# Optimization experiments

Hardware: AMD Instinct MI355X
Metric: run time of the kernel (lower is better)

Reference implementation:

```python
import jax, jax.numpy as jnp
import numpy as np

H = 512  # hidden_size


def _xavier(key, shape):
    fan_out, fan_in = shape[0], shape[1]
    bound = jnp.sqrt(6.0 / (fan_in + fan_out)).astype(jnp.float32)
    return jax.random.uniform(key, shape, jnp.float32, -bound, bound)


def setup_inputs() -> dict:
    key = jax.random.key(0)
    ks = jax.random.split(key, 8)
    B, T, D = 256, 256, 64
    x = jax.random.normal(ks[0], (B, T, D), jnp.float32)
    # LSTM params, PyTorch layout: W_ih [4H, in], W_hh [4H, H], gate order i,f,g,o.
    # biases are zero-initialized in the module; b = b_ih + b_hh folded into one.
    W_ih_0 = _xavier(ks[1], (4 * H, D))
    W_hh_0 = _xavier(ks[2], (4 * H, H))
    b_0 = jnp.zeros((4 * H,), jnp.float32)
    W_ih_1 = _xavier(ks[3], (4 * H, H))
    W_hh_1 = _xavier(ks[4], (4 * H, H))
    b_1 = jnp.zeros((4 * H,), jnp.float32)
    # heads (PyTorch Linear default init: uniform(-1/sqrt(fan_in), 1/sqrt(fan_in)))
    def lin(k, out_f, in_f):
        kw, kb = jax.random.split(k)
        bound = 1.0 / np.sqrt(in_f)
        W = jax.random.uniform(kw, (out_f, in_f), jnp.float32, -bound, bound)
        b = jax.random.uniform(kb, (out_f,), jnp.float32, -bound, bound)
        return W, b
    W_sh, b_sh = lin(ks[5], H // 2, H)
    W_dir, b_dir = lin(ks[6], 1, H // 2)
    W_mag, b_mag = lin(ks[7], 1, H // 2)
    return {
        "x": x,
        "W_ih_0": W_ih_0, "W_hh_0": W_hh_0, "b_0": b_0,
        "W_ih_1": W_ih_1, "W_hh_1": W_hh_1, "b_1": b_1,
        "W_sh": W_sh, "b_sh": b_sh,
        "W_dir": W_dir, "b_dir": b_dir,
        "W_mag": W_mag, "b_mag": b_mag,
    }


def _lstm_layer(x, W_ih, W_hh, b):
    # x: [B, T, D] -> h_seq: [B, T, H]. Input projection batched over time.
    B = x.shape[0]
    xW = jnp.einsum('btd,gd->btg', x, W_ih) + b  # [B, T, 4H]
    xW = jnp.swapaxes(xW, 0, 1)                  # [T, B, 4H]

    def step(carry, xt):
        h, c = carry
        gates = xt + h @ W_hh.T                  # [B, 4H]
        i, f, g, o = jnp.split(gates, 4, axis=-1)
        i = jax.nn.sigmoid(i)
        f = jax.nn.sigmoid(f)
        g = jnp.tanh(g)
        o = jax.nn.sigmoid(o)
        c = f * c + i * g
        h = o * jnp.tanh(c)
        return (h, c), h

    h0 = jnp.zeros((B, H), x.dtype)
    c0 = jnp.zeros((B, H), x.dtype)
    _, h_seq = jax.lax.scan(step, (h0, c0), xW)  # [T, B, H]
    return jnp.swapaxes(h_seq, 0, 1)             # [B, T, H]


def reference(x, W_ih_0, W_hh_0, b_0, W_ih_1, W_hh_1, b_1,
              W_sh, b_sh, W_dir, b_dir, W_mag, b_mag):
    h1 = _lstm_layer(x, W_ih_0, W_hh_0, b_0)   # layer 0
    h2 = _lstm_layer(h1, W_ih_1, W_hh_1, b_1)  # layer 1 (dropout=0 / eval)
    last_hidden = jnp.mean(h2, axis=1)          # mean over time [B, H]
    out = jax.nn.relu(last_hidden @ W_sh.T + b_sh) * 1.5
    direction = out @ W_dir.T + b_dir           # [B, 1]
    magnitude = out @ W_mag.T + b_mag           # [B, 1]
    return (direction, magnitude)
```

## Files before the change

kernel.cpp:

```cpp
#include <hip/hip_runtime.h>
#include <hip/hip_bf16.h>

typedef __attribute__((ext_vector_type(8))) short v8s;
typedef __attribute__((ext_vector_type(4))) float v4f;

static_assert(sizeof(v8s) == 16, "v8s must be 16B");

constexpr int BATCH = 256;
constexpr int SEQT  = 256;
constexpr int HID   = 512;
constexpr int NSLICES = 64;
constexpr int KBH  = 16;
constexpr int KBI0 = 2;
constexpr int KBT0 = KBH + KBI0;
constexpr int KBI1 = 16;
constexpr int KBT1 = KBH + KBI1;
constexpr int BH   = BATCH * HID;


__device__ inline short f2bf(float f) {
    union { __hip_bfloat16 h; short s; } u;
    u.h = __float2bfloat16(f);
    return u.s;
}
__device__ inline float sigf(float x) { return 1.0f / (1.0f + __expf(-x)); }
__device__ inline float tanhf_fast(float x) { return 1.0f - 2.0f / (__expf(2.0f * x) + 1.0f); }

__device__ inline void ld16_wait(const void* p, v8s a[16]) {
    asm volatile(
        "global_load_dwordx4 %0, %16, off sc1\n\t"
        "global_load_dwordx4 %1, %16, off offset:64 sc1\n\t"
        "global_load_dwordx4 %2, %16, off offset:128 sc1\n\t"
        "global_load_dwordx4 %3, %16, off offset:192 sc1\n\t"
        "global_load_dwordx4 %4, %16, off offset:256 sc1\n\t"
        "global_load_dwordx4 %5, %16, off offset:320 sc1\n\t"
        "global_load_dwordx4 %6, %16, off offset:384 sc1\n\t"
        "global_load_dwordx4 %7, %16, off offset:448 sc1\n\t"
        "global_load_dwordx4 %8, %16, off offset:512 sc1\n\t"
        "global_load_dwordx4 %9, %16, off offset:576 sc1\n\t"
        "global_load_dwordx4 %10, %16, off offset:640 sc1\n\t"
        "global_load_dwordx4 %11, %16, off offset:704 sc1\n\t"
        "global_load_dwordx4 %12, %16, off offset:768 sc1\n\t"
        "global_load_dwordx4 %13, %16, off offset:832 sc1\n\t"
        "global_load_dwordx4 %14, %16, off offset:896 sc1\n\t"
        "global_load_dwordx4 %15, %16, off offset:960 sc1\n\t"
        "s_waitcnt vmcnt(0)"
        : "=&v"(a[0]), "=&v"(a[1]), "=&v"(a[2]), "=&v"(a[3]),
          "=&v"(a[4]), "=&v"(a[5]), "=&v"(a[6]), "=&v"(a[7]),
          "=&v"(a[8]), "=&v"(a[9]), "=&v"(a[10]), "=&v"(a[11]),
          "=&v"(a[12]), "=&v"(a[13]), "=&v"(a[14]), "=&v"(a[15])
        : "v"(p) : "memory");
}

__device__ inline void ld16_issue(const void* p, v8s a[16]) {
    asm volatile(
        "global_load_dwordx4 %0, %16, off sc1\n\t"
        "global_load_dwordx4 %1, %16, off offset:64 sc1\n\t"
        "global_load_dwordx4 %2, %16, off offset:128 sc1\n\t"
        "global_load_dwordx4 %3, %16, off offset:192 sc1\n\t"
        "global_load_dwordx4 %4, %16, off offset:256 sc1\n\t"
        "global_load_dwordx4 %5, %16, off offset:320 sc1\n\t"
        "global_load_dwordx4 %6, %16, off offset:384 sc1\n\t"
        "global_load_dwordx4 %7, %16, off offset:448 sc1\n\t"
        "global_load_dwordx4 %8, %16, off offset:512 sc1\n\t"
        "global_load_dwordx4 %9, %16, off offset:576 sc1\n\t"
        "global_load_dwordx4 %10, %16, off offset:640 sc1\n\t"
        "global_load_dwordx4 %11, %16, off offset:704 sc1\n\t"
        "global_load_dwordx4 %12, %16, off offset:768 sc1\n\t"
        "global_load_dwordx4 %13, %16, off offset:832 sc1\n\t"
        "global_load_dwordx4 %14, %16, off offset:896 sc1\n\t"
        "global_load_dwordx4 %15, %16, off offset:960 sc1"
        : "=&v"(a[0]), "=&v"(a[1]), "=&v"(a[2]), "=&v"(a[3]),
          "=&v"(a[4]), "=&v"(a[5]), "=&v"(a[6]), "=&v"(a[7]),
          "=&v"(a[8]), "=&v"(a[9]), "=&v"(a[10]), "=&v"(a[11]),
          "=&v"(a[12]), "=&v"(a[13]), "=&v"(a[14]), "=&v"(a[15])
        : "v"(p) : "memory");
}

__device__ inline void wait_vm0_bind(v8s a[16]) {
    asm volatile("s_waitcnt vmcnt(0)"
        : "+v"(a[0]), "+v"(a[1]), "+v"(a[2]), "+v"(a[3]),
          "+v"(a[4]), "+v"(a[5]), "+v"(a[6]), "+v"(a[7]),
          "+v"(a[8]), "+v"(a[9]), "+v"(a[10]), "+v"(a[11]),
          "+v"(a[12]), "+v"(a[13]), "+v"(a[14]), "+v"(a[15])
        :: "memory");
    __builtin_amdgcn_sched_barrier(0);
}

__device__ inline void st16(void* p, v8s v) {
    asm volatile("global_store_dwordx4 %0, %1, off sc1" :: "v"(p), "v"(v) : "memory");
}

__device__ inline int frags_not_ready(const v8s f[16]) {
    unsigned acc = 0xFFFFFFFFu;
#pragma unroll
    for (int kb = 0; kb < 16; ++kb) {
        union { v8s v; unsigned u[4]; } q; q.v = f[kb];
#pragma unroll
        for (int j = 0; j < 4; ++j) {
            unsigned tw = q.u[j] ^ 0xAAAAAAAAu;
            acc = (tw < acc) ? tw : acc;
        }
    }
    return acc == 0u;
}

__device__ inline void cell_update(const v4f& acc0, const v4f& acc1,
                                   float bi, float bf_, float bg_, float bo,
                                   bool lowhalf, float c[4], float hval[4]) {
    v4f sw0, sw1;
#pragma unroll
    for (int r = 0; r < 4; ++r) {
        sw0[r] = __shfl_xor(acc0[r], 8, 64);
        sw1[r] = __shfl_xor(acc1[r], 8, 64);
    }
#pragma unroll
    for (int r = 0; r < 4; ++r) {
        float ig = (lowhalf ? acc0[r] : sw0[r]) + bi;
        float fg = (lowhalf ? sw0[r] : acc0[r]) + bf_;
        float gg = (lowhalf ? acc1[r] : sw1[r]) + bg_;
        float og = (lowhalf ? sw1[r] : acc1[r]) + bo;
        float cv = sigf(fg) * c[r] + sigf(ig) * tanhf_fast(gg);
        c[r] = cv;
        hval[r] = sigf(og) * tanhf_fast(cv);
    }
}

__global__ __launch_bounds__(256, 1)
void lstm_fused(const float* __restrict__ x,
                const float* __restrict__ Wih0, const float* __restrict__ Whh0,
                const float* __restrict__ bias0,
                const float* __restrict__ Wih1, const float* __restrict__ Whh1,
                const float* __restrict__ bias1,
                float* mean_out,
                __hip_bfloat16* h0seq,
                __hip_bfloat16* ring4)
{
    __shared__ v8s ldsB0[2 * KBT0 * 64];
    __shared__ v8s ldsB1[2 * KBT1 * 64];
    __shared__ alignas(16) short stage[4][16][8];

    const int tid   = threadIdx.x;
    const int lane  = tid & 63;
    const int wv    = tid >> 6;
    const int slice = blockIdx.x & (NSLICES - 1);
    const int bg    = blockIdx.x >> 6;
    const int j0    = slice * 8;
    const int b0    = bg * 64;

    for (int idx = tid; idx < 2 * KBT0 * 64; idx += 256) {
        int tile = idx / (KBT0 * 64);
        int rem  = idx - tile * (KBT0 * 64);
        int kb   = rem >> 6;
        int ls   = rem & 63;
        int n    = tile * 16 + (ls & 15);
        int kh   = ls >> 4;
        int col  = (n >> 3) * 512 + j0 + (n & 7);
        int k    = kb * 32 + kh * 8;
        const float* src = (k < 512) ? (Whh0 + col * 512 + k)
                                     : (Wih0 + col * 64 + (k - 512));
        float4 f0 = ((const float4*)src)[0];
        float4 f1 = ((const float4*)src)[1];
        v8s b;
        b[0]=f2bf(f0.x); b[1]=f2bf(f0.y); b[2]=f2bf(f0.z); b[3]=f2bf(f0.w);
        b[4]=f2bf(f1.x); b[5]=f2bf(f1.y); b[6]=f2bf(f1.z); b[7]=f2bf(f1.w);
        ldsB0[idx] = b;
    }
    for (int idx = tid; idx < 2 * KBT1 * 64; idx += 256) {
        int tile = idx / (KBT1 * 64);
        int rem  = idx - tile * (KBT1 * 64);
        int kb   = rem >> 6;
        int ls   = rem & 63;
        int n    = tile * 16 + (ls & 15);
        int kh   = ls >> 4;
        int col  = (n >> 3) * 512 + j0 + (n & 7);
        int k    = kb * 32 + kh * 8;
        const float* src = (k < 512) ? (Whh1 + col * 512 + k)
                                     : (Wih1 + col * 512 + (k - 512));
        float4 f0 = ((const float4*)src)[0];
        float4 f1 = ((const float4*)src)[1];
        v8s b;
        b[0]=f2bf(f0.x); b[1]=f2bf(f0.y); b[2]=f2bf(f0.z); b[3]=f2bf(f0.w);
        b[4]=f2bf(f1.x); b[5]=f2bf(f1.y); b[6]=f2bf(f1.z); b[7]=f2bf(f1.w);
        ldsB1[idx] = b;
    }
    __syncthreads();

    const int m_a  = b0 + wv * 16 + (lane & 15);
    const int kh8  = (lane >> 4) * 8;
    const int jj   = lane & 7;
    const bool lowhalf = (lane & 8) == 0;
    const int rg   = lane >> 4;

    const float bi0 = bias0[0 * 512 + j0 + jj];
    const float bf0 = bias0[1 * 512 + j0 + jj];
    const float bg0 = bias0[2 * 512 + j0 + jj];
    const float bo0 = bias0[3 * 512 + j0 + jj];
    const float bi1 = bias1[0 * 512 + j0 + jj];
    const float bf1 = bias1[1 * 512 + j0 + jj];
    const float bg1 = bias1[2 * 512 + j0 + jj];
    const float bo1 = bias1[3 * 512 + j0 + jj];

    float c0[4]   = {0.f, 0.f, 0.f, 0.f};
    float c1[4]   = {0.f, 0.f, 0.f, 0.f};
    float hsum[4] = {0.f, 0.f, 0.f, 0.f};

    v8s pz;
#pragma unroll
    for (int i = 0; i < 8; ++i) pz[i] = (short)0xAAAA;

    for (int t = 0; t <= SEQT; ++t) {
        const bool doL0  = (t < SEQT);
        const int  s     = t - 1;
        const bool doL1  = (t > 0);
        const bool doL1r = doL1 && (s > 0);

        if (doL1 && lane < 16) {
            int bcell = b0 + wv * 16 + lane;
            st16(ring4 + (size_t)(t & 3) * BH + bcell * HID + j0, pz);
        }

        v8s fA0[16];
        const int tm1 = (t > 0) ? t - 1 : 0;
        const __hip_bfloat16* hp = h0seq + (size_t)tm1 * BH + m_a * HID + kh8;
        if (t > 0) ld16_issue(hp, fA0);

        v4f a00 = {0.f,0.f,0.f,0.f}, a01 = {0.f,0.f,0.f,0.f};
        if (doL0) {
#pragma unroll
            for (int kb = 0; kb < KBI0; ++kb) {
                const float* xp = x + (m_a * SEQT + t) * 64 + kb * 32 + kh8;
                float4 f0 = ((const float4*)xp)[0];
                float4 f1 = ((const float4*)xp)[1];
                v8s a;
                a[0]=f2bf(f0.x); a[1]=f2bf(f0.y); a[2]=f2bf(f0.z); a[3]=f2bf(f0.w);
                a[4]=f2bf(f1.x); a[5]=f2bf(f1.y); a[6]=f2bf(f1.z); a[7]=f2bf(f1.w);
                a00 = __builtin_amdgcn_mfma_f32_16x16x32_bf16(a, ldsB0[(KBH + kb) * 64 + lane], a00, 0, 0, 0);
                a01 = __builtin_amdgcn_mfma_f32_16x16x32_bf16(a, ldsB0[(KBT0 + KBH + kb) * 64 + lane], a01, 0, 0, 0);
            }
        }

        if (t > 0) {
            wait_vm0_bind(fA0);
            while (__any(frags_not_ready(fA0))) {
                __builtin_amdgcn_s_sleep(1);
                ld16_wait(hp, fA0);
            }
        }

        if (doL0) {
            if (t > 0) {
#pragma unroll
                for (int kb = 0; kb < KBH; ++kb) {
                    a00 = __builtin_amdgcn_mfma_f32_16x16x32_bf16(fA0[kb], ldsB0[kb * 64 + lane], a00, 0, 0, 0);
                    a01 = __builtin_amdgcn_mfma_f32_16x16x32_bf16(fA0[kb], ldsB0[(KBT0 + kb) * 64 + lane], a01, 0, 0, 0);
                }
            }
            float hval[4];
            cell_update(a00, a01, bi0, bf0, bg0, bo0, lowhalf, c0, hval);
            if (lowhalf) {
#pragma unroll
                for (int r = 0; r < 4; ++r)
                    stage[wv][rg * 4 + r][jj] = f2bf(hval[r]);
            }
            asm volatile("s_waitcnt lgkmcnt(0)" ::: "memory");
            if (lane < 16) {
                v8s row = *(const v8s*)(&stage[wv][lane][0]);
                int bcell = b0 + wv * 16 + lane;
                st16(h0seq + (size_t)t * BH + bcell * HID + j0, row);
            }
        }

        if (doL1) {
            v8s fA2[16];
            const __hip_bfloat16* rp = ring4 + (size_t)((s + 3) & 3) * BH + m_a * HID + kh8;
            if (doL1r) ld16_issue(rp, fA2);

            v4f a10 = {0.f,0.f,0.f,0.f}, a11 = {0.f,0.f,0.f,0.f};
#pragma unroll
            for (int kb = 0; kb < KBI1; ++kb) {
                a10 = __builtin_amdgcn_mfma_f32_16x16x32_bf16(fA0[kb], ldsB1[(KBH + kb) * 64 + lane], a10, 0, 0, 0);
                a11 = __builtin_amdgcn_mfma_f32_16x16x32_bf16(fA0[kb], ldsB1[(KBT1 + KBH + kb) * 64 + lane], a11, 0, 0, 0);
            }
            if (doL1r) {
                wait_vm0_bind(fA2);
                while (__any(frags_not_ready(fA2))) {
                    __builtin_amdgcn_s_sleep(1);
                    ld16_wait(rp, fA2);
                }
#pragma unroll
                for (int kb = 0; kb < KBH; ++kb) {
                    a10 = __builtin_amdgcn_mfma_f32_16x16x32_bf16(fA2[kb], ldsB1[kb * 64 + lane], a10, 0, 0, 0);
                    a11 = __builtin_amdgcn_mfma_f32_16x16x32_bf16(fA2[kb], ldsB1[(KBT1 + kb) * 64 + lane], a11, 0, 0, 0);
                }
            }
            float hval[4];
            cell_update(a10, a11, bi1, bf1, bg1, bo1, lowhalf, c1, hval);
#pragma unroll
            for (int r = 0; r < 4; ++r) hsum[r] += hval[r];
            if (lowhalf) {
#pragma unroll
                for (int r = 0; r < 4; ++r)
                    stage[wv][rg * 4 + r][jj] = f2bf(hval[r]);
            }
            asm volatile("s_waitcnt lgkmcnt(0)" ::: "memory");
            if (lane < 16) {
                int bcell = b0 + wv * 16 + lane;
                v8s row = *(const v8s*)(&stage[wv][lane][0]);
                st16(ring4 + (size_t)(s & 3) * BH + bcell * HID + j0, row);
            }
        }
    }

    if (lowhalf) {
        char* mb = (char*)mean_out;
#pragma unroll
        for (int r = 0; r < 4; ++r) {
            int bcell = b0 + wv * 16 + rg * 4 + r;
            int j = j0 + jj;
            float* dst = (float*)(mb + (size_t)(j >> 8) * 262144
                                     + (size_t)bcell * 1024 + (j & 255) * 4);
            *dst = hsum[r] * (1.0f / (float)SEQT);
        }
    }
}

__global__ __launch_bounds__(256)
void head_kernel(const float* __restrict__ mean_h,
                 const float* __restrict__ W_sh, const float* __restrict__ b_sh,
                 const float* __restrict__ W_dir, const float* __restrict__ b_dir,
                 const float* __restrict__ W_mag, const float* __restrict__ b_mag,
                 float* __restrict__ out)
{
    __shared__ float mh[512];
    __shared__ float red[256];
    const int b = blockIdx.x;
    const int tid = threadIdx.x;

    const char* mb = (const char*)mean_h;
    mh[tid]       = *(const float*)(mb + (size_t)b * 1024 + tid * 4);
    mh[tid + 256] = *(const float*)(mb + 262144 + (size_t)b * 1024 + tid * 4);
    __syncthreads();

    const float4* wrow = (const float4*)(W_sh + tid * 512);
    float dot = 0.f;
#pragma unroll 4
    for (int k4 = 0; k4 < 128; ++k4) {
        float4 w = wrow[k4];
        dot += w.x * mh[k4 * 4] + w.y * mh[k4 * 4 + 1]
             + w.z * mh[k4 * 4 + 2] + w.w * mh[k4 * 4 + 3];
    }
    float o = fmaxf(dot + b_sh[tid], 0.f) * 1.5f;

    red[tid] = o * W_dir[tid];
    __syncthreads();
    for (int s = 128; s > 0; s >>= 1) {
        if (tid < s) red[tid] += red[tid + s];
        __syncthreads();
    }
    if (tid == 0) out[b] = red[0] + b_dir[0];
    __syncthreads();

    red[tid] = o * W_mag[tid];
    __syncthreads();
    for (int s = 128; s > 0; s >>= 1) {
        if (tid < s) red[tid] += red[tid + s];
        __syncthreads();
    }
    if (tid == 0) out[256 + b] = red[0] + b_mag[0];
}

extern "C" void kernel_launch(void* const* d_in, const int* in_sizes, int n_in,
                              void* d_out, int out_size, void* d_ws, size_t ws_size,
                              hipStream_t stream) {
    const float* x    = (const float*)d_in[0];
    const float* Wih0 = (const float*)d_in[1];
    const float* Whh0 = (const float*)d_in[2];
    const float* b0   = (const float*)d_in[3];
    const float* Wih1 = (const float*)d_in[4];
    const float* Whh1 = (const float*)d_in[5];
    const float* b1   = (const float*)d_in[6];
    const float* Wsh  = (const float*)d_in[7];
    const float* bsh  = (const float*)d_in[8];
    const float* Wdir = (const float*)d_in[9];
    const float* bdir = (const float*)d_in[10];
    const float* Wmag = (const float*)d_in[11];
    const float* bmag = (const float*)d_in[12];

    char* ws = (char*)d_ws;
    __hip_bfloat16* ring4 = (__hip_bfloat16*)(ws);
    __hip_bfloat16* h0seq = (__hip_bfloat16*)(ws + 1048576);
    float* mean_h         = (float*)(ws + 1048576);


    lstm_fused<<<dim3(256), dim3(256), 0, stream>>>(
        x, Wih0, Whh0, b0, Wih1, Whh1, b1,
        mean_h, h0seq, ring4);
    head_kernel<<<dim3(256), dim3(256), 0, stream>>>(
        mean_h, Wsh, bsh, Wdir, bdir, Wmag, bmag, (float*)d_out);
}
```

Before: 1.462 ms.

## Prefetch next-step layer-0 hidden state and x inputs at end of iteration

```diff
diff --git a/kernel.cpp b/kernel.cpp
--- a/kernel.cpp
+++ b/kernel.cpp
@@ -209,29 +209,48 @@
 #pragma unroll
     for (int i = 0; i < 8; ++i) pz[i] = (short)0xAAAA;
 
+    v8s fP[16];
+    float4 xf[4];
+
+#pragma unroll
+    for (int kb = 0; kb < KBI0; ++kb) {
+        const float* xp = x + (m_a * SEQT + 0) * 64 + kb * 32 + kh8;
+        xf[kb * 2 + 0] = ((const float4*)xp)[0];
+        xf[kb * 2 + 1] = ((const float4*)xp)[1];
+    }
+
     for (int t = 0; t <= SEQT; ++t) {
         const bool doL0  = (t < SEQT);
         const int  s     = t - 1;
         const bool doL1  = (t > 0);
         const bool doL1r = doL1 && (s > 0);
 
-        if (doL1 && lane < 16) {
+        const __hip_bfloat16* hp = h0seq + (size_t)((t > 0) ? t - 1 : 0) * BH
+                                   + m_a * HID + kh8;
+        if (t > 0) {
+            wait_vm0_bind(fP);
+            while (__any(frags_not_ready(fP))) {
+                __builtin_amdgcn_s_sleep(1);
+                ld16_wait(hp, fP);
+            }
+        }
+
+        if (doL1 && doL0 && lane < 16) {
             int bcell = b0 + wv * 16 + lane;
             st16(ring4 + (size_t)(t & 3) * BH + bcell * HID + j0, pz);
         }
 
-        v8s fA0[16];
-        const int tm1 = (t > 0) ? t - 1 : 0;
-        const __hip_bfloat16* hp = h0seq + (size_t)tm1 * BH + m_a * HID + kh8;
-        if (t > 0) ld16_issue(hp, fA0);
+        v8s fA2[16];
+        const __hip_bfloat16* rp = ring4 + (size_t)((s + 3) & 3) * BH
+                                   + m_a * HID + kh8;
+        if (doL1r) ld16_issue(rp, fA2);
 
         v4f a00 = {0.f,0.f,0.f,0.f}, a01 = {0.f,0.f,0.f,0.f};
         if (doL0) {
 #pragma unroll
             for (int kb = 0; kb < KBI0; ++kb) {
-                const float* xp = x + (m_a * SEQT + t) * 64 + kb * 32 + kh8;
-                float4 f0 = ((const float4*)xp)[0];
-                float4 f1 = ((const float4*)xp)[1];
+                float4 f0 = xf[kb * 2 + 0];
+                float4 f1 = xf[kb * 2 + 1];
                 v8s a;
                 a[0]=f2bf(f0.x); a[1]=f2bf(f0.y); a[2]=f2bf(f0.z); a[3]=f2bf(f0.w);
                 a[4]=f2bf(f1.x); a[5]=f2bf(f1.y); a[6]=f2bf(f1.z); a[7]=f2bf(f1.w);
@@ -240,20 +259,12 @@
             }
         }
 
-        if (t > 0) {
-            wait_vm0_bind(fA0);
-            while (__any(frags_not_ready(fA0))) {
-                __builtin_amdgcn_s_sleep(1);
-                ld16_wait(hp, fA0);
-            }
-        }
-
         if (doL0) {
             if (t > 0) {
 #pragma unroll
                 for (int kb = 0; kb < KBH; ++kb) {
-                    a00 = __builtin_amdgcn_mfma_f32_16x16x32_bf16(fA0[kb], ldsB0[kb * 64 + lane], a00, 0, 0, 0);
-                    a01 = __builtin_amdgcn_mfma_f32_16x16x32_bf16(fA0[kb], ldsB0[(KBT0 + kb) * 64 + lane], a01, 0, 0, 0);
+                    a00 = __builtin_amdgcn_mfma_f32_16x16x32_bf16(fP[kb], ldsB0[kb * 64 + lane], a00, 0, 0, 0);
+                    a01 = __builtin_amdgcn_mfma_f32_16x16x32_bf16(fP[kb], ldsB0[(KBT0 + kb) * 64 + lane], a01, 0, 0, 0);
                 }
             }
             float hval[4];
@@ -272,15 +283,11 @@
         }
 
         if (doL1) {
-            v8s fA2[16];
-            const __hip_bfloat16* rp = ring4 + (size_t)((s + 3) & 3) * BH + m_a * HID + kh8;
-            if (doL1r) ld16_issue(rp, fA2);
-
             v4f a10 = {0.f,0.f,0.f,0.f}, a11 = {0.f,0.f,0.f,0.f};
 #pragma unroll
             for (int kb = 0; kb < KBI1; ++kb) {
-                a10 = __builtin_amdgcn_mfma_f32_16x16x32_bf16(fA0[kb], ldsB1[(KBH + kb) * 64 + lane], a10, 0, 0, 0);
-                a11 = __builtin_amdgcn_mfma_f32_16x16x32_bf16(fA0[kb], ldsB1[(KBT1 + KBH + kb) * 64 + lane], a11, 0, 0, 0);
+                a10 = __builtin_amdgcn_mfma_f32_16x16x32_bf16(fP[kb], ldsB1[(KBH + kb) * 64 + lane], a10, 0, 0, 0);
+                a11 = __builtin_amdgcn_mfma_f32_16x16x32_bf16(fP[kb], ldsB1[(KBT1 + KBH + kb) * 64 + lane], a11, 0, 0, 0);
             }
             if (doL1r) {
                 wait_vm0_bind(fA2);
@@ -308,6 +315,18 @@
                 int bcell = b0 + wv * 16 + lane;
                 v8s row = *(const v8s*)(&stage[wv][lane][0]);
                 st16(ring4 + (size_t)(s & 3) * BH + bcell * HID + j0, row);
+            }
+        }
+
+        if (doL0) {
+            ld16_issue(h0seq + (size_t)t * BH + m_a * HID + kh8, fP);
+            if (t + 1 < SEQT) {
+#pragma unroll
+                for (int kb = 0; kb < KBI0; ++kb) {
+                    const float* xp = x + (m_a * SEQT + (t + 1)) * 64 + kb * 32 + kh8;
+                    xf[kb * 2 + 0] = ((const float4*)xp)[0];
+                    xf[kb * 2 + 1] = ((const float4*)xp)[1];
+                }
             }
         }
     }
```

New measurement: 1.916 ms. 31.0% more time.
